# Optimization experiments

Measured on AMD Instinct MI355X. Metric: run time of the kernel, lower is better.

The kernel has to match this reference:

```python
import jax, jax.numpy as jnp
import numpy as np

TEMPERATURE = 0.07
EPS = 1e-12  # F.normalize eps


def setup_inputs() -> dict:
    key = jax.random.key(0)
    k1, k2 = jax.random.split(key)
    features = jax.random.normal(k1, (16, 512, 768), dtype=jnp.float32)
    labels = jax.random.randint(k2, (16, 512), 0, 10, dtype=jnp.int64)
    return {"features": features, "labels": labels}


def reference(features, labels):
    B, S, H = features.shape
    x = features.reshape(-1, H)                       # [N, H], N = B*S
    lab = labels.reshape(-1)                          # [N]
    # F.normalize(dim=-1): divide by clamped L2 norm
    norm = jnp.maximum(jnp.linalg.norm(x, axis=-1, keepdims=True), EPS)
    x = x / norm
    sim = jnp.matmul(x, x.T) / TEMPERATURE            # [N, N]
    label_mask = (lab[None, :] == lab[:, None]).astype(sim.dtype)  # [N, N]
    n_pos = jnp.sum(label_mask)
    n_neg = label_mask.size - n_pos
    # masked means (equivalent to sim[mask].mean() / sim[~mask].mean())
    pos_mean = jnp.sum(sim * label_mask) / n_pos
    neg_mean = (jnp.sum(sim) - jnp.sum(sim * label_mask)) / n_neg
    # -log(exp(p) / (exp(p) + exp(n))) == logaddexp(0, n - p)
    loss = jnp.logaddexp(jnp.zeros((), sim.dtype), neg_mean - pos_mean)
    return loss
```

## Files before the change

### kernel.cpp

```cpp
#include <hip/hip_runtime.h>
#include <math.h>


#define NCLS 10
#define HDIM 768
#define HV4  (HDIM / 4)
#define CLS_FLOATS (NCLS * HDIM)
#define CLS_F4 (CLS_FLOATS / 4)
#define HD_F4  (HDIM / 4)
#define PBLK 256
#define RPB  32
#define K2BLK 24
#define K2THR 512

__global__ __launch_bounds__(768) void k1_fused(
    const float* __restrict__ x, const int* __restrict__ lab,
    float* __restrict__ partials) {
  __shared__ float srn[RPB];
  __shared__ int   slab[RPB];
  const int tid = threadIdx.x, lane = tid & 63, wave = tid >> 6;
  const int row0 = blockIdx.x * RPB;
  const float4* __restrict__ x4 = (const float4*)x;

  for (int r = wave; r < RPB; r += 12) {
    const int row = row0 + r;
    const size_t b = (size_t)row * HV4;
    const float4 t0 = x4[b + lane];
    const float4 t1 = x4[b + 64 + lane];
    const float4 t2 = x4[b + 128 + lane];
    float ss = t0.x * t0.x + t0.y * t0.y + t0.z * t0.z + t0.w * t0.w +
               t1.x * t1.x + t1.y * t1.y + t1.z * t1.z + t1.w * t1.w +
               t2.x * t2.x + t2.y * t2.y + t2.z * t2.z + t2.w * t2.w;
#pragma unroll
    for (int off = 32; off >= 1; off >>= 1) ss += __shfl_xor(ss, off, 64);
    if (lane == 0) {
      srn[r] = 1.0f / fmaxf(sqrtf(ss), 1e-12f);
      slab[r] = lab[row];
    }
  }
  __syncthreads();

  float acc[NCLS];
#pragma unroll
  for (int c = 0; c < NCLS; ++c) acc[c] = 0.0f;

  for (int rb = 0; rb < RPB; rb += 8) {
    float v[8];
#pragma unroll
    for (int u = 0; u < 8; ++u)
      v[u] = x[(size_t)(row0 + rb + u) * HDIM + tid];
#pragma unroll
    for (int u = 0; u < 8; ++u) {
      const float s = srn[rb + u];
      const int c = __builtin_amdgcn_readfirstlane(slab[rb + u]);
      const float p = v[u] * s;
      switch (c) {
        case 0: acc[0] += p; break;
        case 1: acc[1] += p; break;
        case 2: acc[2] += p; break;
        case 3: acc[3] += p; break;
        case 4: acc[4] += p; break;
        case 5: acc[5] += p; break;
        case 6: acc[6] += p; break;
        case 7: acc[7] += p; break;
        case 8: acc[8] += p; break;
        default: acc[9] += p; break;
      }
    }
  }

  float* __restrict__ outp = partials + (size_t)blockIdx.x * CLS_FLOATS;
#pragma unroll
  for (int c = 0; c < NCLS; ++c) outp[c * HDIM + tid] = acc[c];
}

__global__ __launch_bounds__(K2THR) void k2_full(
    const float* __restrict__ partials, double* __restrict__ bsums) {
  const float4* __restrict__ p4 = (const float4*)partials;
  const int tid = threadIdx.x, lane = tid & 63, wave = tid >> 6;
  const int f  = tid & 7;
  const int pg = tid >> 3;
  const int h04 = blockIdx.x * 8;

  float4 acc[NCLS];
#pragma unroll
  for (int c = 0; c < NCLS; ++c) acc[c] = make_float4(0.f, 0.f, 0.f, 0.f);

  const size_t base = (size_t)(pg * 4) * CLS_F4 + (size_t)h04 + f;
#pragma unroll
  for (int pp = 0; pp < 4; ++pp) {
#pragma unroll
    for (int c = 0; c < NCLS; ++c) {
      const float4 v = p4[base + (size_t)pp * CLS_F4 + c * HD_F4];
      acc[c].x += v.x; acc[c].y += v.y; acc[c].z += v.z; acc[c].w += v.w;
    }
  }

#pragma unroll
  for (int c = 0; c < NCLS; ++c) {
#pragma unroll
    for (int off = 8; off <= 32; off <<= 1) {
      acc[c].x += __shfl_xor(acc[c].x, off, 64);
      acc[c].y += __shfl_xor(acc[c].y, off, 64);
      acc[c].z += __shfl_xor(acc[c].z, off, 64);
      acc[c].w += __shfl_xor(acc[c].w, off, 64);
    }
  }

  __shared__ float4 sred[K2THR / 64][NCLS][8];
  if (lane < 8) {
#pragma unroll
    for (int c = 0; c < NCLS; ++c) sred[wave][c][lane] = acc[c];
  }
  __syncthreads();

  __shared__ float4 sS[NCLS][8];
  if (tid < NCLS * 8) {
    const int c = tid >> 3, ff = tid & 7;
    float4 s = sred[0][c][ff];
#pragma unroll
    for (int w = 1; w < K2THR / 64; ++w) {
      const float4 v = sred[w][c][ff];
      s.x += v.x; s.y += v.y; s.z += v.z; s.w += v.w;
    }
    sS[c][ff] = s;
  }
  __syncthreads();

  __shared__ double smm[8], stt[8];
  if (tid < 8) {
    double m = 0.0, t0 = 0.0, t1 = 0.0, t2 = 0.0, t3 = 0.0;
#pragma unroll
    for (int c = 0; c < NCLS; ++c) {
      const float4 s = sS[c][tid];
      m += (double)s.x * s.x + (double)s.y * s.y +
           (double)s.z * s.z + (double)s.w * s.w;
      t0 += s.x; t1 += s.y; t2 += s.z; t3 += s.w;
    }
    smm[tid] = m;
    stt[tid] = t0 * t0 + t1 * t1 + t2 * t2 + t3 * t3;
  }
  __syncthreads();
  if (tid == 0) {
    double m = 0.0, t = 0.0;
#pragma unroll
    for (int i = 0; i < 8; ++i) { m += smm[i]; t += stt[i]; }
    bsums[(size_t)blockIdx.x * 2]     = m;
    bsums[(size_t)blockIdx.x * 2 + 1] = t;
  }
}

__global__ __launch_bounds__(512) void k3_final(
    const double* __restrict__ bsums, const int* __restrict__ lab,
    float* __restrict__ out, int N) {
  __shared__ int scnt[NCLS];
  const int tid = threadIdx.x, lane = tid & 63;
  if (tid < NCLS) scnt[tid] = 0;
  __syncthreads();

  int cnt[NCLS];
#pragma unroll
  for (int c = 0; c < NCLS; ++c) cnt[c] = 0;
  for (int i = tid; i < N; i += blockDim.x) {
    const int l = lab[i];
#pragma unroll
    for (int c = 0; c < NCLS; ++c) cnt[c] += (l == c);
  }
#pragma unroll
  for (int c = 0; c < NCLS; ++c) {
    int v = cnt[c];
#pragma unroll
    for (int off = 32; off >= 1; off >>= 1) v += __shfl_xor(v, off, 64);
    if (lane == 0) atomicAdd(&scnt[c], v);
  }
  __syncthreads();

  if (tid == 0) {
    double m = 0.0, t = 0.0;
#pragma unroll
    for (int b = 0; b < K2BLK; ++b) {
      m += bsums[2 * b];
      t += bsums[2 * b + 1];
    }
    double n_pos = 0.0;
    for (int c = 0; c < NCLS; ++c) { const double cc = scnt[c]; n_pos += cc * cc; }
    const double T = 0.07;
    const double nn = (double)N * (double)N;
    const double pos_mean = m / (T * n_pos);
    const double neg_mean = (t - m) / (T * (nn - n_pos));
    const double d = neg_mean - pos_mean;
    out[0] = (float)(fmax(d, 0.0) + log1p(exp(-fabs(d))));
  }
}

extern "C" void kernel_launch(void* const* d_in, const int* in_sizes, int n_in,
                              void* d_out, int out_size, void* d_ws, size_t ws_size,
                              hipStream_t stream) {
  const float* x = (const float*)d_in[0];
  const int* lab = (const int*)d_in[1];
  const int N = in_sizes[1];

  float* partials = (float*)d_ws;
  double* bsums = (double*)(partials + (size_t)PBLK * CLS_FLOATS);

  k1_fused<<<PBLK, HDIM, 0, stream>>>(x, lab, partials);
  k2_full<<<K2BLK, K2THR, 0, stream>>>(partials, bsums);
  k3_final<<<1, 512, 0, stream>>>(bsums, lab, (float*)d_out, N);
}
```

Baseline: 89.25 us.

## Fuse reduction and final kernels via cooperative launch with grid sync

```diff
diff --git a/kernel.cpp b/kernel.cpp
--- a/kernel.cpp
+++ b/kernel.cpp
@@ -1,5 +1,8 @@
 #include <hip/hip_runtime.h>
+#include <hip/hip_cooperative_groups.h>
 #include <math.h>
+
+namespace cg = cooperative_groups;
 
 
 #define NCLS 10
@@ -74,8 +77,10 @@
   for (int c = 0; c < NCLS; ++c) outp[c * HDIM + tid] = acc[c];
 }
 
-__global__ __launch_bounds__(K2THR) void k2_full(
-    const float* __restrict__ partials, double* __restrict__ bsums) {
+__global__ __launch_bounds__(K2THR) void k23_fused(
+    const float* __restrict__ partials, const int* __restrict__ lab,
+    double* __restrict__ bsums, int* __restrict__ bcnt,
+    float* __restrict__ out, int N) {
   const float4* __restrict__ p4 = (const float4*)partials;
   const int tid = threadIdx.x, lane = tid & 63, wave = tid >> 6;
   const int f  = tid & 7;
@@ -140,7 +145,13 @@
     smm[tid] = m;
     stt[tid] = t0 * t0 + t1 * t1 + t2 * t2 + t3 * t3;
   }
-  __syncthreads();
+
+  __shared__ int shc[NCLS];
+  if (tid < NCLS) shc[tid] = 0;
+  __syncthreads();
+  const int gi = blockIdx.x * K2THR + tid;
+  if (gi < N) atomicAdd(&shc[lab[gi]], 1);
+
   if (tid == 0) {
     double m = 0.0, t = 0.0;
 #pragma unroll
@@ -148,42 +159,31 @@
     bsums[(size_t)blockIdx.x * 2]     = m;
     bsums[(size_t)blockIdx.x * 2 + 1] = t;
   }
-}
-
-__global__ __launch_bounds__(512) void k3_final(
-    const double* __restrict__ bsums, const int* __restrict__ lab,
-    float* __restrict__ out, int N) {
-  __shared__ int scnt[NCLS];
-  const int tid = threadIdx.x, lane = tid & 63;
-  if (tid < NCLS) scnt[tid] = 0;
-  __syncthreads();
-
-  int cnt[NCLS];
-#pragma unroll
-  for (int c = 0; c < NCLS; ++c) cnt[c] = 0;
-  for (int i = tid; i < N; i += blockDim.x) {
-    const int l = lab[i];
-#pragma unroll
-    for (int c = 0; c < NCLS; ++c) cnt[c] += (l == c);
-  }
-#pragma unroll
-  for (int c = 0; c < NCLS; ++c) {
-    int v = cnt[c];
-#pragma unroll
-    for (int off = 32; off >= 1; off >>= 1) v += __shfl_xor(v, off, 64);
-    if (lane == 0) atomicAdd(&scnt[c], v);
-  }
-  __syncthreads();
-
-  if (tid == 0) {
+  __syncthreads();
+  if (tid < NCLS) bcnt[blockIdx.x * NCLS + tid] = shc[tid];
+
+  cg::this_grid().sync();
+
+  if (blockIdx.x == 0 && tid == 0) {
     double m = 0.0, t = 0.0;
 #pragma unroll
     for (int b = 0; b < K2BLK; ++b) {
       m += bsums[2 * b];
       t += bsums[2 * b + 1];
     }
+    int cnt[NCLS];
+#pragma unroll
+    for (int c = 0; c < NCLS; ++c) cnt[c] = 0;
+    for (int b = 0; b < K2BLK; ++b) {
+#pragma unroll
+      for (int c = 0; c < NCLS; ++c) cnt[c] += bcnt[b * NCLS + c];
+    }
     double n_pos = 0.0;
-    for (int c = 0; c < NCLS; ++c) { const double cc = scnt[c]; n_pos += cc * cc; }
+#pragma unroll
+    for (int c = 0; c < NCLS; ++c) {
+      const double cc = (double)cnt[c];
+      n_pos += cc * cc;
+    }
     const double T = 0.07;
     const double nn = (double)N * (double)N;
     const double pos_mean = m / (T * n_pos);
@@ -202,8 +202,18 @@
 
   float* partials = (float*)d_ws;
   double* bsums = (double*)(partials + (size_t)PBLK * CLS_FLOATS);
+  int* bcnt = (int*)(bsums + 2 * K2BLK);
 
   k1_fused<<<PBLK, HDIM, 0, stream>>>(x, lab, partials);
-  k2_full<<<K2BLK, K2THR, 0, stream>>>(partials, bsums);
-  k3_final<<<1, 512, 0, stream>>>(bsums, lab, (float*)d_out, N);
+
+  const float* p_partials = partials;
+  const int*   p_lab = lab;
+  double*      p_bsums = bsums;
+  int*         p_bcnt = bcnt;
+  float*       p_out = (float*)d_out;
+  int          p_N = N;
+  void* args[] = {(void*)&p_partials, (void*)&p_lab, (void*)&p_bsums,
+                  (void*)&p_bcnt, (void*)&p_out, (void*)&p_N};
+  hipLaunchCooperativeKernel(reinterpret_cast<void*>(k23_fused),
+                             dim3(K2BLK), dim3(K2THR), args, 0, stream);
 }
```

Result: slower. 106.5 us (+19.4%).
